# Kernel tuning notes

Hardware: AMD Instinct MI355X
Metric: run time of the kernel (lower is better)

Reference implementation:

```python
import jax, jax.numpy as jnp
import numpy as np

B, H, W, IN, HID, L, M1, M2, OUT, NT = 32, 128, 256, 4, 64, 4, 12, 12, 2, 14


def setup_inputs() -> dict:
    key = jax.random.key(0)
    ks = jax.random.split(key, 32)
    f32 = jnp.float32
    n = lambda k, s, scale=0.02: jax.random.normal(k, s, dtype=f32) * scale
    inp = jax.random.normal(ks[0], (B, H, W, IN), dtype=f32)
    # ext: [B,1,6]; col0 float feature, col2 day idx in [0,8), col3 hour idx in [5,19)
    c0 = jax.random.uniform(ks[1], (B, 1), dtype=f32)
    c1 = jax.random.uniform(ks[2], (B, 1), dtype=f32)
    c2 = jax.random.randint(ks[3], (B, 1), 0, 8).astype(f32)
    c3 = jax.random.randint(ks[4], (B, 1), 5, 19).astype(f32)
    c45 = jax.random.uniform(ks[5], (B, 2), dtype=f32)
    ext = jnp.concatenate([c0, c1, c2, c3, c45], axis=1)[:, None, :]
    return {
        'inp': inp, 'ext': ext,
        'enc_w': n(ks[6], (HID, IN + 1)), 'enc_b': n(ks[7], (HID,)),
        'w1r': n(ks[8], (L, HID, HID, M1, M2), 1.0 / (HID * HID)),
        'w1i': n(ks[9], (L, HID, HID, M1, M2), 1.0 / (HID * HID)),
        'w2r': n(ks[10], (L, HID, HID, M1, M2), 1.0 / (HID * HID)),
        'w2i': n(ks[11], (L, HID, HID, M1, M2), 1.0 / (HID * HID)),
        'ws_w': n(ks[12], (L, HID, HID)), 'ws_b': n(ks[13], (L, HID)),
        'day_emb': n(ks[14], (8, 2), 1.0), 'hour_emb': n(ks[15], (24, 3), 1.0),
        'e1_w': n(ks[16], (64, 6)), 'e1_b': n(ks[17], (64,)),
        'e2_w': n(ks[18], (H * W, 64)), 'e2_b': n(ks[19], (H * W,)),
        'tw': n(ks[20], (NT, HID, HID, 3, 3)), 'tb': n(ks[21], (NT, HID)),
        'f1_w': n(ks[22], (128, HID)), 'f1_b': n(ks[23], (128,)),
        'f2_w': n(ks[24], (HID, 128)), 'f2_b': n(ks[25], (HID,)),
        'f3_w': n(ks[26], (OUT, HID)), 'f3_b': n(ks[27], (OUT,)),
    }


def _act(x):
    return jax.nn.gelu(x, approximate=False)  # torch nn.GELU default (erf)


def _spectral(x, w1, w2):
    # x: [b,c,h,w]; w1,w2: complex [c_in,c_out,M1,M2]
    b, c, h, w = x.shape
    xft = jnp.fft.rfft2(x)  # [b,c,h,w//2+1]
    out = jnp.zeros((b, w1.shape[1], h, w // 2 + 1), dtype=xft.dtype)
    out = out.at[:, :, :M1, :M2].set(
        jnp.einsum('bixy,ioxy->boxy', xft[:, :, :M1, :M2], w1))
    out = out.at[:, :, -M1:, :M2].set(
        jnp.einsum('bixy,ioxy->boxy', xft[:, :, -M1:, :M2], w2))
    return jnp.fft.irfft2(out, s=(h, w))


def reference(inp, ext, enc_w, enc_b, w1r, w1i, w2r, w2i, ws_w, ws_b,
              day_emb, hour_emb, e1_w, e1_b, e2_w, e2_b, tw, tb,
              f1_w, f1_b, f2_w, f2_b, f3_w, f3_b):
    b, h, w, _ = inp.shape
    e = ext[:, 0, :]  # squeeze(1) -> [b,6]
    # embed_ext: [ext0, day_emb, hour_emb] -> [b,6]
    emb = jnp.concatenate([
        e[:, 0:1],
        day_emb[e[:, 2].astype(jnp.int32)],
        hour_emb[e[:, 3].astype(jnp.int32)],
    ], axis=1)
    # ext2lr_global (dropout = identity in eval)
    g = _act(emb @ e1_w.T + e1_b)
    g = _act(g @ e2_w.T + e2_b).reshape(b, h, w, 1)
    x = jnp.concatenate([inp, g], axis=-1)          # [b,h,w,IN+1]
    x = (x @ enc_w.T + enc_b).transpose(0, 3, 1, 2)  # [b,HID,h,w]
    # FNO integral layers
    for i in range(L):
        x1 = _spectral(x, w1r[i] + 1j * w1i[i], w2r[i] + 1j * w2i[i])
        x2 = jnp.einsum('bchw,oc->bohw', x, ws_w[i]) + ws_b[i][None, :, None, None]
        x = x1 + x2
        if i != L - 1:
            x = _act(x)
    # decoder_time: per-sample expert conv selected by hour index
    t = e[:, 3].astype(jnp.int32) - 5  # in [0, NT)
    Wt, bt = tw[t], tb[t]              # [b,HID,HID,3,3], [b,HID]
    def one(xi, wi, bi):
        y = jax.lax.conv_general_dilated(
            xi[None], wi, (1, 1), 'SAME',
            dimension_numbers=('NCHW', 'OIHW', 'NCHW'))[0]
        return y + bi[:, None, None]
    hfeat = _act(jax.vmap(one)(x, Wt, bt)).transpose(0, 2, 3, 1)  # [b,h,w,HID]
    # decoder MLP
    z = _act(hfeat @ f1_w.T + f1_b)
    z = _act(z @ f2_w.T + f2_b)
    return z @ f3_w.T + f3_b  # [b,h,w,OUT]
```

## Files before the change

kernel.cpp:

```cpp
#include <hip/hip_runtime.h>
#include <math.h>

#define BB 32
#define HH_ 128
#define WW_ 256

typedef _Float16 f16_t;
typedef _Float16 half8 __attribute__((ext_vector_type(8)));
typedef _Float16 half4 __attribute__((ext_vector_type(4)));
typedef _Float16 half2v __attribute__((ext_vector_type(2)));
typedef float floatx4 __attribute__((ext_vector_type(4)));

__device__ __forceinline__ float gelu_f(float v){
  float av = __builtin_fabsf(v);
  float s = av * 0.70710678118654752f;
  float k = __builtin_amdgcn_rcpf(__builtin_fmaf(0.3275911f, s, 1.0f));
  float p = __builtin_fmaf(1.061405429f, k, -1.453152027f);
  p = __builtin_fmaf(p, k, 1.421413741f);
  p = __builtin_fmaf(p, k, -0.284496736f);
  p = __builtin_fmaf(p, k, 0.254829592f);
  p = p * k;
  float e = __expf(-s * s);
  float q = 0.5f * av * p;
  return __builtin_fmaf(-q, e, fmaxf(v, 0.f));
}

__global__ void k_diag(float* out, float v){ out[threadIdx.x] = v; }

__global__ __launch_bounds__(256) void k_prep(
      float2* twf, float2* thf, float2* thi, f16_t* twzh,
      const float* __restrict__ f1_w, const float* __restrict__ f2_w,
      const float* __restrict__ f3_w, f16_t* f1T, f16_t* f2T, f16_t* f3T,
      const float* __restrict__ tw, f16_t* __restrict__ wT,
      const float* __restrict__ w1r, const float* __restrict__ w1i,
      const float* __restrict__ w2r, const float* __restrict__ w2i,
      float2* __restrict__ wmix, f16_t* __restrict__ twA){
  __shared__ __align__(16) char smp[53248];
  const double PI2 = 6.283185307179586476925286766559;
  int blk = blockIdx.x, tid = threadIdx.x;
  if (blk < 113){
    int t = blk*256 + tid;
    if (t < 3072){
      int w = t/12, ky = t%12;
      double a = -PI2 * (double)(w*ky) / 256.0;
      twf[t] = make_float2((float)cos(a), (float)sin(a));
    } else if (t < 6144){
      int f = t-3072; int h = f/24, j = f%24;
      int kx = (j<12)? j : j+104;
      double a = -PI2 * (double)(h*kx) / 128.0;
      thf[f] = make_float2((float)cos(a), (float)sin(a));
    } else if (t < 9216){
      int f = t-6144; int h = f/24, j = f%24;
      int kx = (j<12)? j : j+104;
      double a = PI2 * (double)(h*kx) / 128.0;
      thi[f] = make_float2((float)(cos(a)/128.0), (float)(sin(a)/128.0));
    } else if (t < 12288){
      int f = t-9216; int w = f/12, ky = f%12;
      double a = PI2 * (double)(w*ky) / 256.0;
      double s = (ky==0)? 1.0 : 2.0;
      twzh[w*32 + ky]      = (f16_t)( s*cos(a)/256.0);
      twzh[w*32 + 12 + ky] = (f16_t)(-s*sin(a)/256.0);
      if (ky < 8) twzh[w*32 + 24 + ky] = (f16_t)0.f;
    } else {
      int t2 = t - 12288;
      if (t2 < 8192) f1T[t2] = (f16_t)f1_w[t2];
      else if (t2 < 16384) f2T[t2-8192] = (f16_t)f2_w[t2-8192];
      else if (t2 < 16512) f3T[t2-16384] = (f16_t)f3_w[t2-16384];
    }
  } else if (blk < 169){
    float* s = (float*)smp;
    int b2 = blk - 113;
    int og = b2 & 3, tt = b2 >> 2;
    const float* src = tw + (long)tt*36864 + og*9216;
    for (int f = tid; f < 9216; f += 256) s[f] = src[f];
    __syncthreads();
    for (int f = tid; f < 9216; f += 256){
      int c = f & 63; int r = f >> 6;
      int o16 = r % 16, tap = r / 16;
      float v = s[(o16*64 + c)*9 + tap];
      wT[(((long)tt*9 + tap)*64 + og*16 + o16)*64 + c] = (f16_t)v;
    }
  } else if (blk < 937){
    float* sr = (float*)smp;
    float* si = (float*)(smp + 26624);
    int b2 = blk - 169;
    int ig  = b2 & 7;
    int kx  = (b2 >> 3) % 12;
    int sel = (b2 / 96) & 1;
    int l   = b2 / 192;
    const float* wr = sel ? w2r : w1r;
    const float* wi = sel ? w2i : w1i;
    for (int f = tid; f < 6144; f += 256){
      int i8 = f / 768; int rem = f % 768;
      int o = rem / 12, ky = rem % 12;
      long addr = (((long)l*64 + ig*8 + i8)*64 + o)*144 + kx*12 + ky;
      sr[(i8*64 + o)*13 + ky] = wr[addr];
      si[(i8*64 + o)*13 + ky] = wi[addr];
    }
    __syncthreads();
    int j = sel ? (kx + 12) : kx;
    for (int f = tid; f < 6144; f += 256){
      int o = f & 63; int r = f >> 6;
      int ky = r % 12, i8 = r / 12;
      int sidx = (i8*64 + o)*13 + ky;
      wmix[(((long)l*288 + j*12 + ky))*4096 + (ig*8 + i8)*64 + o] =
          make_float2(sr[sidx], si[sidx]);
    }
  } else {
    int t = (blk - 937)*256 + tid;
    int halfi = t >> 13, r = t & 8191;
    int hl = r >> 12, r2 = r & 4095;
    int m = r2 >> 7, k = r2 & 127;
    f16_t v = (f16_t)0.f;
    if (m < 24){
      int ky = m >> 1, ri = m & 1;
      int w = halfi*128 + k;
      double a = -PI2 * (double)(w*ky) / 256.0;
      float t32 = (float)(ri ? sin(a) : cos(a));
      f16_t hi = (f16_t)t32;
      v = hl ? (f16_t)(t32 - (float)hi) : hi;
    }
    twA[t] = v;
  }
}

__global__ __launch_bounds__(256) void k_gxdft(const float* __restrict__ ext,
      const float* __restrict__ day_emb, const float* __restrict__ hour_emb,
      const float* __restrict__ e1_w, const float* __restrict__ e1_b,
      const float* __restrict__ e2_w, const float* __restrict__ e2_b,
      const float* __restrict__ inp, const float* __restrict__ enc_w,
      const float* __restrict__ enc_b, const f16_t* __restrict__ twA,
      f16_t* __restrict__ x, float2* __restrict__ fp0, float2* __restrict__ fp1){
  __shared__ __align__(16) char sm[41984];
  f16_t* Obt   = (f16_t*)sm;
  float* gvs   = (float*)(sm + 35072);
  float4* ips  = (float4*)(sm + 36096);
  float* s     = (float*)(sm + 40192);
  float* ew    = (float*)(sm + 40448);
  float* eb    = (float*)(sm + 41728);
  int tid = threadIdx.x;
  int bh = blockIdx.x;
  int b = bh >> 7, h = bh & 127;
  if (tid < 64){
    int j = tid;
    const float* e = ext + b*6;
    float emb[6];
    emb[0] = e[0];
    int d  = (int)e[2];
    emb[1] = day_emb[d*2];  emb[2] = day_emb[d*2+1];
    int hr = (int)e[3];
    emb[3] = hour_emb[hr*3]; emb[4] = hour_emb[hr*3+1]; emb[5] = hour_emb[hr*3+2];
    float acc = e1_b[j];
    #pragma unroll
    for (int k = 0; k < 6; k++) acc += emb[k]*e1_w[j*6+k];
    s[j] = gelu_f(acc);
    eb[j] = enc_b[j];
  }
  for (int f = tid; f < 320; f += 256) ew[f] = enc_w[f];
  __syncthreads();
  {
    int px = tid;
    long hw = (long)h*256 + px;
    const float4* wrow = (const float4*)(e2_w + hw*64);
    float acc = e2_b[hw];
    #pragma unroll
    for (int k = 0; k < 16; k++){
      float4 v = wrow[k];
      acc += v.x*s[4*k] + v.y*s[4*k+1] + v.z*s[4*k+2] + v.w*s[4*k+3];
    }
    gvs[px] = gelu_f(acc);
    ips[px] = *(const float4*)(inp + ((long)b*32768 + hw)*4);
  }
  __syncthreads();
  int lane = tid & 63, wv = tid >> 6;
  {
    int c = lane, wg = wv;
    const float* wr2 = ew + c*5;
    float w0 = wr2[0], w1 = wr2[1], w2 = wr2[2], w3 = wr2[3], w4 = wr2[4];
    float ebc = eb[c];
    f16_t* xo = x + ((long)bh*256 + wg*64)*64 + c;
    #pragma unroll 2
    for (int g8 = 0; g8 < 8; g8++){
      half8 hv;
      #pragma unroll
      for (int e2 = 0; e2 < 8; e2++){
        int i = g8*8 + e2;
        float4 ip = ips[wg*64 + i];
        float gv = gvs[wg*64 + i];
        float v = ebc + ip.x*w0 + ip.y*w1 + ip.z*w2 + ip.w*w3 + gv*w4;
        f16_t hval = (f16_t)v;
        hv[e2] = hval;
        xo[i*64] = hval;
      }
      *(half8*)(Obt + c*274 + wg*64 + g8*8) = hv;
    }
  }
  __syncthreads();
  int n15 = lane & 15, quad = lane >> 4;
  int n = wv*16 + n15;
  #pragma unroll
  for (int half = 0; half < 2; half++){
    half8 bfr2[4];
    #pragma unroll
    for (int ks = 0; ks < 4; ks++)
      bfr2[ks] = *(const half8*)(Obt + n*274 + half*128 + ks*32 + quad*8);
    floatx4 dacc[2];
    dacc[0] = (floatx4){0.f,0.f,0.f,0.f};
    dacc[1] = (floatx4){0.f,0.f,0.f,0.f};
    #pragma unroll
    for (int hl = 0; hl < 2; hl++){
      #pragma unroll
      for (int mt = 0; mt < 2; mt++){
        #pragma unroll
        for (int ks = 0; ks < 4; ks++){
          half8 a = *(const half8*)(twA + half*8192 + hl*4096
                                    + (mt*16 + n15)*128 + ks*32 + quad*8);
          dacc[mt] = __builtin_amdgcn_mfma_f32_16x16x32_f16(a, bfr2[ks],
                                                            dacc[mt], 0,0,0);
        }
      }
    }
    float2* dst = half ? fp1 : fp0;
    #pragma unroll
    for (int mt = 0; mt < 2; mt++){
      int m0 = mt*16 + quad*4;
      if (m0 < 24){
        int ky0 = m0 >> 1;
        dst[(long)bh*768 + ky0*64 + n]     = make_float2(dacc[mt][0], dacc[mt][1]);
        dst[(long)bh*768 + (ky0+1)*64 + n] = make_float2(dacc[mt][2], dacc[mt][3]);
      }
    }
  }
}

__global__ __launch_bounds__(256) void k_spec(const float2* __restrict__ s0,
      const float2* __restrict__ s1, int dual, const float2* __restrict__ thf_g,
      const float2* __restrict__ thi_g, const float2* __restrict__ wmix,
      int layer, float2* __restrict__ zi){
  __shared__ __align__(16) char sm[40960];
  float2* th  = (float2*)sm;
  float2* xch = (float2*)(sm + 24576);
  float2* mixL= (float2*)(sm + 24576);
  int tid = threadIdx.x;
  int b = blockIdx.x / 12, ky = blockIdx.x % 12;
  int wv = tid >> 6, lane = tid & 63;
  for (int f = tid; f < 3072; f += 256) th[f] = thf_g[f];
  float2 acc[6];
  #pragma unroll
  for (int q = 0; q < 6; q++) acc[q] = make_float2(0.f, 0.f);
  long base = (long)b*98304 + ky*64;
  for (int ch = 0; ch < 4; ch++){
    __syncthreads();
    for (int f = tid; f < 2048; f += 256){
      int hh = f >> 6, c = f & 63;
      long idx = base + (long)(ch*32 + hh)*768 + c;
      float2 v = s0[idx];
      if (dual){ float2 u = s1[idx]; v.x += u.x; v.y += u.y; }
      xch[f] = v;
    }
    __syncthreads();
    for (int hh = 0; hh < 32; hh++){
      float2 v = xch[hh*64 + lane];
      int hg = ch*32 + hh;
      #pragma unroll
      for (int q = 0; q < 6; q++){
        float2 t = th[hg*24 + q*4 + wv];
        acc[q].x += t.x*v.x - t.y*v.y;
        acc[q].y += t.x*v.y + t.y*v.x;
      }
    }
  }
  __syncthreads();
  for (int f = tid; f < 3072; f += 256) th[f] = thi_g[f];
  float2 mout[6];
  #pragma unroll
  for (int q = 0; q < 6; q++){
    int j = q*4 + wv;
    const float2* wj = wmix + (((long)layer*288 + j*12 + ky))*4096;
    float re = 0.f, im = 0.f;
    #pragma unroll 8
    for (int i = 0; i < 64; i++){
      float vr = __shfl(acc[q].x, i);
      float vi = __shfl(acc[q].y, i);
      float2 ww = wj[i*64 + lane];
      re += vr*ww.x - vi*ww.y;
      im += vr*ww.y + vi*ww.x;
    }
    mout[q] = make_float2(re, im);
  }
  #pragma unroll
  for (int q = 0; q < 6; q++) mixL[(q*4 + wv)*64 + lane] = mout[q];
  __syncthreads();
  float2 cr[24];
  #pragma unroll
  for (int j = 0; j < 24; j++) cr[j] = mixL[j*64 + lane];
  for (int qq = 0; qq < 32; qq++){
    int h = qq*4 + wv;
    float re = 0.f, im = 0.f;
    #pragma unroll
    for (int j = 0; j < 24; j++){
      float2 t = th[h*24 + j];
      re += t.x*cr[j].x - t.y*cr[j].y;
      im += t.x*cr[j].y + t.y*cr[j].x;
    }
    zi[((long)b*128 + h)*768 + ky*64 + lane] = make_float2(re, im);
  }
}

__global__ __launch_bounds__(256) void k_iw_mfma(f16_t* __restrict__ x,
      const float2* __restrict__ zi, const float* __restrict__ ws_w,
      const float* __restrict__ ws_b, const f16_t* __restrict__ twzh,
      const f16_t* __restrict__ twA, float2* __restrict__ fp0,
      float2* __restrict__ fp1, int layer, int act, int dodft){
  __shared__ __align__(16) char sm[28672];
  f16_t* A1  = (f16_t*)sm;
  f16_t* Bzh = (f16_t*)(sm + 18432);
  f16_t* Bzl = (f16_t*)(sm + 23552);
  f16_t* Obt = (f16_t*)sm;
  int tid = threadIdx.x;
  int blk = blockIdx.x;
  int half = blk & 1;
  long bh = blk >> 1;
  int w0 = half*128;
  const f16_t* xrow = x + (bh*256 + w0)*64;
  for (int f = tid; f < 1024; f += 256){
    int px = f >> 3, c8 = f & 7;
    *(float4*)(A1 + px*72 + c8*8) = *(const float4*)(xrow + px*64 + c8*8);
  }
  const float2* zrow = zi + bh*768;
  for (int f = tid; f < 768; f += 256){
    int o = f & 63, ky = f >> 6;
    float2 v = zrow[ky*64 + o];
    f16_t hr = (f16_t)v.x; f16_t hi_ = (f16_t)v.y;
    Bzh[o*40 + ky]      = hr;
    Bzh[o*40 + 12 + ky] = hi_;
    Bzl[o*40 + ky]      = (f16_t)(v.x - (float)hr);
    Bzl[o*40 + 12 + ky] = (f16_t)(v.y - (float)hi_);
  }
  if (tid < 64){
    float4 z4 = {0.f,0.f,0.f,0.f};
    *(float4*)(Bzh + tid*40 + 24) = z4;
    *(float4*)(Bzl + tid*40 + 24) = z4;
  }
  __syncthreads();
  int lane = tid & 63, wv = tid >> 6;
  int n15 = lane & 15, quad = lane >> 4;
  int n = wv*16 + n15;
  half8 bws[2];
  {
    const float* wsl = ws_w + ((long)layer*64 + n)*64;
    #pragma unroll
    for (int kc = 0; kc < 2; kc++){
      float4 u0 = *(const float4*)(wsl + kc*32 + quad*8);
      float4 u1 = *(const float4*)(wsl + kc*32 + quad*8 + 4);
      half8 hb;
      hb[0]=(f16_t)u0.x; hb[1]=(f16_t)u0.y; hb[2]=(f16_t)u0.z; hb[3]=(f16_t)u0.w;
      hb[4]=(f16_t)u1.x; hb[5]=(f16_t)u1.y; hb[6]=(f16_t)u1.z; hb[7]=(f16_t)u1.w;
      bws[kc] = hb;
    }
  }
  half8 bzh = *(const half8*)(Bzh + n*40 + quad*8);
  half8 bzl = *(const half8*)(Bzl + n*40 + quad*8);
  floatx4 acc[8];
  #pragma unroll
  for (int mt = 0; mt < 8; mt++){
    floatx4 c = {0.f,0.f,0.f,0.f};
    half8 ax0 = *(const half8*)(A1 + (mt*16 + n15)*72 + quad*8);
    half8 ax1 = *(const half8*)(A1 + (mt*16 + n15)*72 + 32 + quad*8);
    half8 atw = *(const half8*)(twzh + (w0 + mt*16 + n15)*32 + quad*8);
    c = __builtin_amdgcn_mfma_f32_16x16x32_f16(ax0, bws[0], c, 0,0,0);
    c = __builtin_amdgcn_mfma_f32_16x16x32_f16(ax1, bws[1], c, 0,0,0);
    c = __builtin_amdgcn_mfma_f32_16x16x32_f16(atw, bzh,    c, 0,0,0);
    c = __builtin_amdgcn_mfma_f32_16x16x32_f16(atw, bzl,    c, 0,0,0);
    acc[mt] = c;
  }
  float bias = ws_b[layer*64 + n];
  __syncthreads();
  f16_t* xo = x + (bh*256 + w0)*64;
  #pragma unroll
  for (int mt = 0; mt < 8; mt++){
    half4 hv;
    #pragma unroll
    for (int r = 0; r < 4; r++){
      float v = acc[mt][r] + bias;
      if (act) v = gelu_f(v);
      hv[r] = (f16_t)v;
      xo[(mt*16 + quad*4 + r)*64 + n] = hv[r];
    }
    if (dodft) *(half4*)(Obt + n*136 + mt*16 + quad*4) = hv;
  }
  if (dodft){
    __syncthreads();
    half8 bfr2[4];
    #pragma unroll
    for (int ks = 0; ks < 4; ks++)
      bfr2[ks] = *(const half8*)(Obt + n*136 + ks*32 + quad*8);
    floatx4 dacc[2];
    dacc[0] = (floatx4){0.f,0.f,0.f,0.f};
    dacc[1] = (floatx4){0.f,0.f,0.f,0.f};
    #pragma unroll
    for (int hl = 0; hl < 2; hl++){
      #pragma unroll
      for (int mt = 0; mt < 2; mt++){
        #pragma unroll
        for (int ks = 0; ks < 4; ks++){
          half8 a = *(const half8*)(twA + half*8192 + hl*4096
                                    + (mt*16 + n15)*128 + ks*32 + quad*8);
          dacc[mt] = __builtin_amdgcn_mfma_f32_16x16x32_f16(a, bfr2[ks],
                                                            dacc[mt], 0,0,0);
        }
      }
    }
    float2* dst = half ? fp1 : fp0;
    #pragma unroll
    for (int mt = 0; mt < 2; mt++){
      int m0 = mt*16 + quad*4;
      if (m0 < 24){
        int ky0 = m0 >> 1;
        dst[bh*768 + ky0*64 + n]     = make_float2(dacc[mt][0], dacc[mt][1]);
        dst[bh*768 + (ky0+1)*64 + n] = make_float2(dacc[mt][2], dacc[mt][3]);
      }
    }
  }
}

__global__ __launch_bounds__(256) void k_conv_head(const f16_t* __restrict__ x,
      const float* __restrict__ ext, const f16_t* __restrict__ wT,
      const float* __restrict__ tb, const f16_t* __restrict__ f1T,
      const float* __restrict__ f1_b, const f16_t* __restrict__ f2T,
      const float* __restrict__ f2_b, const f16_t* __restrict__ f3T,
      const float* __restrict__ f3_b, float* __restrict__ out){
  __shared__ __align__(16) char sm[29824];
  f16_t* hf   = (f16_t*)sm;
  f16_t* z1   = (f16_t*)(sm + 9216);
  f16_t* z2   = (f16_t*)sm;
  float* tbs  = (float*)(sm + 28512);
  float* f1bs = (float*)(sm + 28768);
  float* f2bs = (float*)(sm + 29280);
  f16_t* f3s  = (f16_t*)(sm + 29536);
  float* f3bs = (float*)(sm + 29792);
  f16_t* xt   = (f16_t*)sm;

  int tid = threadIdx.x;
  int blk = blockIdx.x;
  int wc = blk & 3, h = (blk >> 2) & 127, b = blk >> 9;
  int w0 = wc*64;
  int t_idx = (int)ext[b*6+3] - 5;

  if (tid < 64) tbs[tid] = tb[t_idx*64 + tid];
  else if (tid < 192) f1bs[tid-64] = f1_b[tid-64];
  else f2bs[tid-192] = f2_b[tid-192];
  if (tid < 128) f3s[tid] = f3T[tid];
  if (tid < 2) f3bs[tid] = f3_b[tid];

  for (int f = tid; f < 1536; f += 256){
    int c8 = f & 7, px = (f >> 3) & 63, dy = f >> 9;
    int hh = h - 1 + dy;
    float4 v = {0.f,0.f,0.f,0.f};
    if (hh >= 0 && hh < HH_)
      v = *(const float4*)(x + (((long)b*HH_ + hh)*WW_ + w0 + px)*64 + c8*8);
    *(float4*)(xt + (dy*66 + px + 1)*72 + c8*8) = v;
  }
  if (tid < 48){
    int c8 = tid & 7, r = tid >> 3;
    int dy = r >> 1, side = r & 1;
    int pxl = side ? 65 : 0;
    int hh = h - 1 + dy, wg = w0 - 1 + pxl;
    float4 v = {0.f,0.f,0.f,0.f};
    if (hh >= 0 && hh < HH_ && wg >= 0 && wg < WW_)
      v = *(const float4*)(x + (((long)b*HH_ + hh)*WW_ + wg)*64 + c8*8);
    *(float4*)(xt + (dy*66 + pxl)*72 + c8*8) = v;
  }
  __syncthreads();

  int lane = tid & 63, wv = tid >> 6;
  int n15 = lane & 15, quad = lane >> 4;

  floatx4 acc[4];
  #pragma unroll
  for (int mt = 0; mt < 4; mt++) acc[mt] = (floatx4){0.f,0.f,0.f,0.f};
  const f16_t* wTt = wT + (long)t_idx*36864;
  for (int tap = 0; tap < 9; tap++){
    int dy = tap/3, dx = tap%3;
    const f16_t* wrow = wTt + (tap*64 + wv*16 + n15)*64;
    #pragma unroll
    for (int kc = 0; kc < 2; kc++){
      half8 bfrag = *(const half8*)(wrow + kc*32 + quad*8);
      #pragma unroll
      for (int mt = 0; mt < 4; mt++){
        int p = mt*16 + n15 + dx;
        half8 a = *(const half8*)(xt + (dy*66 + p)*72 + kc*32 + quad*8);
        acc[mt] = __builtin_amdgcn_mfma_f32_16x16x32_f16(a, bfrag, acc[mt], 0,0,0);
      }
    }
  }
  __syncthreads();
  {
    int n = wv*16 + n15;
    float bias = tbs[n];
    #pragma unroll
    for (int mt = 0; mt < 4; mt++){
      #pragma unroll
      for (int r = 0; r < 4; r++){
        int m = mt*16 + quad*4 + r;
        hf[m*72 + n] = (f16_t)gelu_f(acc[mt][r] + bias);
      }
    }
  }
  __syncthreads();
  #pragma unroll
  for (int nt = 0; nt < 2; nt++){
    int n = wv*32 + nt*16 + n15;
    float bias = f1bs[n];
    half8 bf0 = *(const half8*)(f1T + n*64 + quad*8);
    half8 bf1 = *(const half8*)(f1T + n*64 + 32 + quad*8);
    #pragma unroll
    for (int mt = 0; mt < 4; mt++){
      floatx4 c = {0.f,0.f,0.f,0.f};
      half8 a0 = *(const half8*)(hf + (mt*16 + n15)*72 + quad*8);
      half8 a1 = *(const half8*)(hf + (mt*16 + n15)*72 + 32 + quad*8);
      c = __builtin_amdgcn_mfma_f32_16x16x32_f16(a0, bf0, c, 0,0,0);
      c = __builtin_amdgcn_mfma_f32_16x16x32_f16(a1, bf1, c, 0,0,0);
      #pragma unroll
      for (int r = 0; r < 4; r++){
        int m = mt*16 + quad*4 + r;
        z1[m*136 + n] = (f16_t)gelu_f(c[r] + bias);
      }
    }
  }
  __syncthreads();
  {
    int n = wv*16 + n15;
    float bias = f2bs[n];
    half8 bf[4];
    #pragma unroll
    for (int kc = 0; kc < 4; kc++)
      bf[kc] = *(const half8*)(f2T + n*128 + kc*32 + quad*8);
    #pragma unroll
    for (int mt = 0; mt < 4; mt++){
      floatx4 c = {0.f,0.f,0.f,0.f};
      #pragma unroll
      for (int kc = 0; kc < 4; kc++){
        half8 a = *(const half8*)(z1 + (mt*16 + n15)*136 + kc*32 + quad*8);
        c = __builtin_amdgcn_mfma_f32_16x16x32_f16(a, bf[kc], c, 0,0,0);
      }
      #pragma unroll
      for (int r = 0; r < 4; r++){
        int m = mt*16 + quad*4 + r;
        z2[m*72 + n] = (f16_t)gelu_f(c[r] + bias);
      }
    }
  }
  __syncthreads();
  if (tid < 128){
    int px = tid >> 1, oo = tid & 1;
    const f16_t* zr = z2 + px*72;
    const f16_t* fr = f3s + oo*64;
    float a = f3bs[oo];
    #pragma unroll
    for (int g = 0; g < 8; g++){
      half8 zv = *(const half8*)(zr + g*8);
      half8 wv2 = *(const half8*)(fr + g*8);
#if __has_builtin(__builtin_amdgcn_fdot2)
      #pragma unroll
      for (int q = 0; q < 4; q++){
        half2v za = {zv[2*q], zv[2*q+1]};
        half2v wa = {wv2[2*q], wv2[2*q+1]};
        a = __builtin_amdgcn_fdot2(za, wa, a, false);
      }
#else
      #pragma unroll
      for (int q = 0; q < 8; q++) a += (float)zv[q]*(float)wv2[q];
#endif
    }
    out[(((long)b*HH_ + h)*WW_ + w0 + px)*2 + oo] = a;
  }
}

extern "C" void kernel_launch(void* const* d_in, const int* in_sizes, int n_in,
                              void* d_out, int out_size, void* d_ws, size_t ws_size,
                              hipStream_t stream){
  const float* inp     = (const float*)d_in[0];
  const float* ext     = (const float*)d_in[1];
  const float* enc_w   = (const float*)d_in[2];
  const float* enc_b   = (const float*)d_in[3];
  const float* w1r     = (const float*)d_in[4];
  const float* w1i     = (const float*)d_in[5];
  const float* w2r     = (const float*)d_in[6];
  const float* w2i     = (const float*)d_in[7];
  const float* ws_w    = (const float*)d_in[8];
  const float* ws_b    = (const float*)d_in[9];
  const float* day_emb = (const float*)d_in[10];
  const float* hour_emb= (const float*)d_in[11];
  const float* e1_w    = (const float*)d_in[12];
  const float* e1_b    = (const float*)d_in[13];
  const float* e2_w    = (const float*)d_in[14];
  const float* e2_b    = (const float*)d_in[15];
  const float* tw      = (const float*)d_in[16];
  const float* tb      = (const float*)d_in[17];
  const float* f1_w    = (const float*)d_in[18];
  const float* f1_b    = (const float*)d_in[19];
  const float* f2_w    = (const float*)d_in[20];
  const float* f2_b    = (const float*)d_in[21];
  const float* f3_w    = (const float*)d_in[22];
  const float* f3_b    = (const float*)d_in[23];
  float* outp = (float*)d_out;

  const size_t need = 248652032;
  if (ws_size < need){
    k_diag<<<dim3(1), dim3(64), 0, stream>>>(outp, (float)(ws_size >> 20));
    return;
  }
  char* p = (char*)d_ws;
  f16_t*  x    = (f16_t*)(p);
  float2* fp0  = (float2*)(p + 134217728);
  float2* fp1  = (float2*)(p + 159383552);
  float2* zi   = (float2*)(p + 184549376);
  float2* twf  = (float2*)(p + 209715200);
  float2* thf  = (float2*)(p + 209739776);
  float2* thi  = (float2*)(p + 209764352);
  f16_t*  twzh = (f16_t*)(p + 209788928);
  f16_t*  wT   = (f16_t*)(p + 209805312);
  f16_t*  f1T  = (f16_t*)(p + 210837504);
  f16_t*  f2T  = (f16_t*)(p + 210853888);
  f16_t*  f3T  = (f16_t*)(p + 210870272);
  float2* wmix = (float2*)(p + 210870528);
  f16_t*  twA  = (f16_t*)(p + 248619264);

  k_prep<<<dim3(1001), dim3(256), 0, stream>>>(twf, thf, thi, twzh,
      f1_w, f2_w, f3_w, f1T, f2T, f3T, tw, wT, w1r, w1i, w2r, w2i, wmix, twA);
  k_gxdft<<<dim3(4096), dim3(256), 0, stream>>>(ext, day_emb, hour_emb,
      e1_w, e1_b, e2_w, e2_b, inp, enc_w, enc_b, twA, x, fp0, fp1);
  for (int l = 0; l < 4; l++){
    k_spec<<<dim3(384), dim3(256), 0, stream>>>(fp0, fp1, 1,
                                                thf, thi, wmix, l, zi);
    k_iw_mfma<<<dim3(8192), dim3(256), 0, stream>>>(x, zi, ws_w, ws_b, twzh,
                       twA, fp0, fp1, l, (l < 3) ? 1 : 0, (l < 3) ? 1 : 0);
  }
  k_conv_head<<<dim3(16384), dim3(256), 0, stream>>>(x, ext, wT, tb,
                     f1T, f1_b, f2T, f2_b, f3T, f3_b, outp);
}
```

Measured before the change: 1.200 ms.

## Widen k_spec to 512 threads and transpose decoder MLP MFMA operand roles

k_spec now runs 8 waves per block instead of 4, so each wave handles 3 instead of 6 of the 24 output rows. This doubles parallelism for a grid of only 384 blocks, which otherwise underfills the GPU. In the conv head, the f1 and f2 MLP MFMAs swap operands so weights are the A matrix and activations the B matrix, letting each lane write 4 contiguous fp16 outputs and load the bias as a float4 instead of doing scattered scalar stores. The cost is more shared-memory traffic per block and heavier register use in k_spec.

```diff
diff --git a/kernel.cpp b/kernel.cpp
--- a/kernel.cpp
+++ b/kernel.cpp
@@ -233,7 +233,7 @@
   }
 }
 
-__global__ __launch_bounds__(256) void k_spec(const float2* __restrict__ s0,
+__global__ __launch_bounds__(512) void k_spec(const float2* __restrict__ s0,
       const float2* __restrict__ s1, int dual, const float2* __restrict__ thf_g,
       const float2* __restrict__ thi_g, const float2* __restrict__ wmix,
       int layer, float2* __restrict__ zi){
@@ -244,14 +244,14 @@
   int tid = threadIdx.x;
   int b = blockIdx.x / 12, ky = blockIdx.x % 12;
   int wv = tid >> 6, lane = tid & 63;
-  for (int f = tid; f < 3072; f += 256) th[f] = thf_g[f];
-  float2 acc[6];
-  #pragma unroll
-  for (int q = 0; q < 6; q++) acc[q] = make_float2(0.f, 0.f);
+  for (int f = tid; f < 3072; f += 512) th[f] = thf_g[f];
+  float2 acc[3];
+  #pragma unroll
+  for (int q = 0; q < 3; q++) acc[q] = make_float2(0.f, 0.f);
   long base = (long)b*98304 + ky*64;
   for (int ch = 0; ch < 4; ch++){
     __syncthreads();
-    for (int f = tid; f < 2048; f += 256){
+    for (int f = tid; f < 2048; f += 512){
       int hh = f >> 6, c = f & 63;
       long idx = base + (long)(ch*32 + hh)*768 + c;
       float2 v = s0[idx];
@@ -263,19 +263,19 @@
       float2 v = xch[hh*64 + lane];
       int hg = ch*32 + hh;
       #pragma unroll
-      for (int q = 0; q < 6; q++){
-        float2 t = th[hg*24 + q*4 + wv];
+      for (int q = 0; q < 3; q++){
+        float2 t = th[hg*24 + q*8 + wv];
         acc[q].x += t.x*v.x - t.y*v.y;
         acc[q].y += t.x*v.y + t.y*v.x;
       }
     }
   }
   __syncthreads();
-  for (int f = tid; f < 3072; f += 256) th[f] = thi_g[f];
-  float2 mout[6];
-  #pragma unroll
-  for (int q = 0; q < 6; q++){
-    int j = q*4 + wv;
+  for (int f = tid; f < 3072; f += 512) th[f] = thi_g[f];
+  float2 mout[3];
+  #pragma unroll
+  for (int q = 0; q < 3; q++){
+    int j = q*8 + wv;
     const float2* wj = wmix + (((long)layer*288 + j*12 + ky))*4096;
     float re = 0.f, im = 0.f;
     #pragma unroll 8
@@ -289,13 +289,13 @@
     mout[q] = make_float2(re, im);
   }
   #pragma unroll
-  for (int q = 0; q < 6; q++) mixL[(q*4 + wv)*64 + lane] = mout[q];
+  for (int q = 0; q < 3; q++) mixL[(q*8 + wv)*64 + lane] = mout[q];
   __syncthreads();
   float2 cr[24];
   #pragma unroll
   for (int j = 0; j < 24; j++) cr[j] = mixL[j*64 + lane];
-  for (int qq = 0; qq < 32; qq++){
-    int h = qq*4 + wv;
+  for (int qq = 0; qq < 16; qq++){
+    int h = qq*8 + wv;
     float re = 0.f, im = 0.f;
     #pragma unroll
     for (int j = 0; j < 24; j++){
@@ -508,47 +508,48 @@
     }
   }
   __syncthreads();
-  #pragma unroll
-  for (int nt = 0; nt < 2; nt++){
-    int n = wv*32 + nt*16 + n15;
-    float bias = f1bs[n];
-    half8 bf0 = *(const half8*)(f1T + n*64 + quad*8);
-    half8 bf1 = *(const half8*)(f1T + n*64 + 32 + quad*8);
-    #pragma unroll
-    for (int mt = 0; mt < 4; mt++){
+  {
+    int px = wv*16 + n15;
+    half8 bhf0 = *(const half8*)(hf + px*72 + quad*8);
+    half8 bhf1 = *(const half8*)(hf + px*72 + 32 + quad*8);
+    #pragma unroll
+    for (int mt2 = 0; mt2 < 8; mt2++){
       floatx4 c = {0.f,0.f,0.f,0.f};
-      half8 a0 = *(const half8*)(hf + (mt*16 + n15)*72 + quad*8);
-      half8 a1 = *(const half8*)(hf + (mt*16 + n15)*72 + 32 + quad*8);
-      c = __builtin_amdgcn_mfma_f32_16x16x32_f16(a0, bf0, c, 0,0,0);
-      c = __builtin_amdgcn_mfma_f32_16x16x32_f16(a1, bf1, c, 0,0,0);
-      #pragma unroll
-      for (int r = 0; r < 4; r++){
-        int m = mt*16 + quad*4 + r;
-        z1[m*136 + n] = (f16_t)gelu_f(c[r] + bias);
-      }
+      half8 a0 = *(const half8*)(f1T + (mt2*16 + n15)*64 + quad*8);
+      half8 a1 = *(const half8*)(f1T + (mt2*16 + n15)*64 + 32 + quad*8);
+      c = __builtin_amdgcn_mfma_f32_16x16x32_f16(a0, bhf0, c, 0,0,0);
+      c = __builtin_amdgcn_mfma_f32_16x16x32_f16(a1, bhf1, c, 0,0,0);
+      float4 b4 = *(const float4*)(f1bs + mt2*16 + quad*4);
+      half4 hv;
+      hv[0] = (f16_t)gelu_f(c[0] + b4.x);
+      hv[1] = (f16_t)gelu_f(c[1] + b4.y);
+      hv[2] = (f16_t)gelu_f(c[2] + b4.z);
+      hv[3] = (f16_t)gelu_f(c[3] + b4.w);
+      *(half4*)(z1 + px*136 + mt2*16 + quad*4) = hv;
     }
   }
   __syncthreads();
   {
-    int n = wv*16 + n15;
-    float bias = f2bs[n];
-    half8 bf[4];
+    int px = wv*16 + n15;
+    half8 bz[4];
     #pragma unroll
     for (int kc = 0; kc < 4; kc++)
-      bf[kc] = *(const half8*)(f2T + n*128 + kc*32 + quad*8);
-    #pragma unroll
-    for (int mt = 0; mt < 4; mt++){
+      bz[kc] = *(const half8*)(z1 + px*136 + kc*32 + quad*8);
+    #pragma unroll
+    for (int mt3 = 0; mt3 < 4; mt3++){
       floatx4 c = {0.f,0.f,0.f,0.f};
       #pragma unroll
       for (int kc = 0; kc < 4; kc++){
-        half8 a = *(const half8*)(z1 + (mt*16 + n15)*136 + kc*32 + quad*8);
-        c = __builtin_amdgcn_mfma_f32_16x16x32_f16(a, bf[kc], c, 0,0,0);
-      }
-      #pragma unroll
-      for (int r = 0; r < 4; r++){
-        int m = mt*16 + quad*4 + r;
-        z2[m*72 + n] = (f16_t)gelu_f(c[r] + bias);
-      }
+        half8 a = *(const half8*)(f2T + (mt3*16 + n15)*128 + kc*32 + quad*8);
+        c = __builtin_amdgcn_mfma_f32_16x16x32_f16(a, bz[kc], c, 0,0,0);
+      }
+      float4 b4 = *(const float4*)(f2bs + mt3*16 + quad*4);
+      half4 hv;
+      hv[0] = (f16_t)gelu_f(c[0] + b4.x);
+      hv[1] = (f16_t)gelu_f(c[1] + b4.y);
+      hv[2] = (f16_t)gelu_f(c[2] + b4.z);
+      hv[3] = (f16_t)gelu_f(c[3] + b4.w);
+      *(half4*)(z2 + px*72 + mt3*16 + quad*4) = hv;
     }
   }
   __syncthreads();
@@ -632,7 +633,7 @@
   k_gxdft<<<dim3(4096), dim3(256), 0, stream>>>(ext, day_emb, hour_emb,
       e1_w, e1_b, e2_w, e2_b, inp, enc_w, enc_b, twA, x, fp0, fp1);
   for (int l = 0; l < 4; l++){
-    k_spec<<<dim3(384), dim3(256), 0, stream>>>(fp0, fp1, 1,
+    k_spec<<<dim3(384), dim3(512), 0, stream>>>(fp0, fp1, 1,
                                                 thf, thi, wmix, l, zi);
     k_iw_mfma<<<dim3(8192), dim3(256), 0, stream>>>(x, zi, ws_w, ws_b, twzh,
                        twA, fp0, fp1, l, (l < 3) ? 1 : 0, (l < 3) ? 1 : 0);
```

New measurement: 1.372 ms. +14.3%, slower.
